# Kernel tuning notes

Hardware: AMD Instinct MI355X
Metric: run time of the kernel (lower is better)

## Reference

```python
import jax, jax.numpy as jnp
import numpy as np

B, L, C, H = 8, 16384, 128, 4
EPS = 1e-5


def setup_inputs() -> dict:
    key = jax.random.key(0)
    k1, k2, k3, k4 = jax.random.split(key, 4)
    return {
        "x": jax.random.normal(k1, (B, L, C), dtype=jnp.float32),
        "W_qkv": jax.random.normal(k2, (3 * C, C), dtype=jnp.float32) * (C ** -0.5),
        "W_out": jax.random.normal(k3, (C, C), dtype=jnp.float32) * (C ** -0.5),
        "b_out": jax.random.normal(k4, (C,), dtype=jnp.float32) * 0.01,
        "gn_w": jnp.ones((C,), dtype=jnp.float32),
        "gn_b": jnp.zeros((C,), dtype=jnp.float32),
    }


def reference(x, W_qkv, W_out, b_out, gn_w, gn_b):
    b, l, c = x.shape
    h = H
    d = c // h                      # dim_head
    scale = d ** -0.5
    xc = jnp.swapaxes(x, 1, 2)      # [b, c, l]
    # 1x1 conv == channel matmul
    qkv = jnp.einsum('oc,bcl->bol', W_qkv, xc)     # [b, 3c, l]
    q, k, v = jnp.split(qkv, 3, axis=1)
    q = q.reshape(b, h, d, l)
    k = k.reshape(b, h, d, l)
    v = v.reshape(b, h, d, l)
    q = jax.nn.softmax(q, axis=2) * scale          # softmax over head-dim
    k = jax.nn.softmax(k, axis=3)                  # softmax over length
    context = jnp.einsum('bhcj,bhdj->bhcd', k, v)  # [b, h, d, d]
    out = jnp.einsum('bhcd,bhdi->bhci', context, q)  # [b, h, d, l]
    out = out.reshape(b, h * d, l)
    out = jnp.einsum('oc,bcl->bol', W_out, out) + b_out[None, :, None]
    # GroupNorm(1, c): normalize over (channel, length) per sample
    mean = jnp.mean(out, axis=(1, 2), keepdims=True)
    var = jnp.var(out, axis=(1, 2), keepdims=True)
    out = (out - mean) * jax.lax.rsqrt(var + EPS)
    out = out * gn_w[None, :, None] + gn_b[None, :, None]
    return jnp.swapaxes(out, 1, 2)                 # [b, l, c]
```

## Files before the change

### kernel.cpp

```cpp
#include <hip/hip_runtime.h>

#define BATCH 8
#define SEQL 16384
#define NCH 128
#define NH 4
#define HD 32
#define GEPS 1e-5f

typedef __bf16 bf16x8 __attribute__((ext_vector_type(8)));
typedef __bf16 bf16x4 __attribute__((ext_vector_type(4)));
typedef float f32x4 __attribute__((ext_vector_type(4)));

#define WKV_B   0
#define WQ_B    65536
#define WO_B    98304
#define CTXB_B  131072
#define GNS_B   196608
#define CTXP_B  262144


__global__ void k_prep(const float* __restrict__ wqkv, const float* __restrict__ wout,
                       char* __restrict__ wsb) {
    int i = blockIdx.x * 256 + threadIdx.x;
    __bf16* wkvb = (__bf16*)(wsb + WKV_B);
    __bf16* wqb  = (__bf16*)(wsb + WQ_B);
    __bf16* wob  = (__bf16*)(wsb + WO_B);
    if (i < 384 * 128) {
        int o = i >> 7, c = i & 127;
        __bf16 v = (__bf16)wqkv[i];
        if (o < 128) wqb[o * 128 + c] = v;
        else         wkvb[(o - 128) * 128 + c] = v;
    }
    if (i < 128 * 128) wob[i] = (__bf16)wout[i];
    if (i < 16) ((float*)(wsb + GNS_B))[i] = 0.f;
}

__global__ __launch_bounds__(256, 4) void k_pass1(const float* __restrict__ x,
                                                  char* __restrict__ wsb, int P) {
    __shared__ __attribute__((aligned(16))) __bf16 xb[8352];
    __shared__ __attribute__((aligned(16))) __bf16 ekv[8232];
    const int t = threadIdx.x;
    const int lane = t & 63, wave = t >> 6;
    const int n16 = lane & 15, q = lane >> 4;
    const int batch = blockIdx.x / P, sub = blockIdx.x % P;
    const int nrep = 256 / P;
    const __bf16* __restrict__ wkvb = (const __bf16*)(wsb + WKV_B);

    f32x4 ctxacc[2][2];
#pragma unroll
    for (int i = 0; i < 2; i++)
#pragma unroll
        for (int j = 0; j < 2; j++) ctxacc[i][j] = (f32x4){0.f, 0.f, 0.f, 0.f};
    float zacc[2][4];
#pragma unroll
    for (int i = 0; i < 2; i++)
#pragma unroll
        for (int j = 0; j < 4; j++) zacc[i][j] = 0.f;

    for (int rep = 0; rep < nrep; rep++) {
        const int chunk = sub + rep * P;
        const float* xg = x + (size_t)(batch * SEQL + chunk * 64) * NCH;
#pragma unroll
        for (int r = 0; r < 8; r++) {
            int e = t + r * 256;
            int tok = e >> 5, c4 = (e & 31) * 4;
            float4 v = ((const float4*)xg)[e];
            bf16x4 h; h.x = (__bf16)v.x; h.y = (__bf16)v.y; h.z = (__bf16)v.z; h.w = (__bf16)v.w;
            *(bf16x4*)&xb[(c4 >> 5) * 2088 + ((c4 >> 3) & 3) * 520 + tok * 8 + (c4 & 7)] = h;
        }
        __syncthreads();

#pragma unroll
        for (int half = 0; half < 2; half++) {
            f32x4 kvacc[4][2];
#pragma unroll
            for (int i = 0; i < 4; i++)
#pragma unroll
                for (int j = 0; j < 2; j++) kvacc[i][j] = (f32x4){0.f, 0.f, 0.f, 0.f};
#pragma unroll
            for (int ks = 0; ks < 4; ks++) {
                bf16x8 aw_k[4];
#pragma unroll
                for (int mt = 0; mt < 4; mt++)
                    aw_k[mt] = *(const bf16x8*)&wkvb[(mt * 64 + wave * 16 + n16) * 128 + ks * 32 + q * 8];
                bf16x8 b[2];
#pragma unroll
                for (int nl = 0; nl < 2; nl++)
                    b[nl] = *(const bf16x8*)&xb[ks * 2088 + q * 520 + ((half * 2 + nl) * 16 + n16) * 8];
#pragma unroll
                for (int mt = 0; mt < 4; mt++)
#pragma unroll
                    for (int nl = 0; nl < 2; nl++)
                        kvacc[mt][nl] = __builtin_amdgcn_mfma_f32_16x16x32_bf16(
                            aw_k[mt], b[nl], kvacc[mt][nl], 0, 0, 0);
            }
#pragma unroll
            for (int mt = 0; mt < 4; mt++)
#pragma unroll
                for (int nl = 0; nl < 2; nl++) {
                    int ti = nl * 16 + n16;
                    int base = (ti >> 3) * 2056 + (ti & 7);
#pragma unroll
                    for (int r = 0; r < 4; r++) {
                        float vv = kvacc[mt][nl][r];
                        if (mt < 2) { vv = __expf(vv); zacc[mt][r] += vv; }
                        int o = mt * 64 + wave * 16 + q * 4 + r;
                        ekv[base + o * 8] = (__bf16)vv;
                    }
                }
            __syncthreads();
            {
                bf16x8 ea[2], vb[2];
#pragma unroll
                for (int ml = 0; ml < 2; ml++) {
                    ea[ml] = *(const bf16x8*)&ekv[q * 2056 + (wave * 32 + ml * 16 + n16) * 8];
                    vb[ml] = *(const bf16x8*)&ekv[q * 2056 + (128 + wave * 32 + ml * 16 + n16) * 8];
                }
#pragma unroll
                for (int ml = 0; ml < 2; ml++)
#pragma unroll
                    for (int nl = 0; nl < 2; nl++)
                        ctxacc[ml][nl] = __builtin_amdgcn_mfma_f32_16x16x32_bf16(
                            ea[ml], vb[nl], ctxacc[ml][nl], 0, 0, 0);
            }
            if (half == 0) __syncthreads();
        }
    }

    float* ctxp = (float*)(wsb + CTXP_B) + (size_t)blockIdx.x * 4096 + wave * 1024;
#pragma unroll
    for (int nl = 0; nl < 2; nl++)
#pragma unroll
        for (int ml = 0; ml < 2; ml++) {
            float4 v4;
            v4.x = ctxacc[ml][nl][0]; v4.y = ctxacc[ml][nl][1];
            v4.z = ctxacc[ml][nl][2]; v4.w = ctxacc[ml][nl][3];
            *(float4*)&ctxp[(nl * 16 + n16) * 32 + ml * 16 + q * 4] = v4;
        }
    {
        float* zpT = (float*)(wsb + CTXP_B) + (size_t)BATCH * P * 4096;
#pragma unroll
        for (int mt = 0; mt < 2; mt++)
#pragma unroll
            for (int r = 0; r < 4; r++) {
                float z = zacc[mt][r];
                z += __shfl_xor(z, 1); z += __shfl_xor(z, 2);
                z += __shfl_xor(z, 4); z += __shfl_xor(z, 8);
                if (n16 == 0)
                    zpT[((size_t)batch * 128 + mt * 64 + wave * 16 + q * 4 + r) * P + sub] = z;
            }
    }
}

__global__ __launch_bounds__(256) void k_reduce(char* __restrict__ wsb, int P) {
    __shared__ float red[4][64];
    __shared__ float zw[32];
    const int tid = threadIdx.x;
    const int b = blockIdx.x >> 6, eg = blockIdx.x & 63;
    const float* ctxp = (const float*)(wsb + CTXP_B);
    const float* zpT = ctxp + (size_t)BATCH * P * 4096;

    {
        int ci = tid >> 3, pslot = tid & 7;
        size_t row = ((size_t)b * 128 + (size_t)(eg >> 4) * 32 + ci) * P;
        float zs = 0.f;
        for (int p = pslot; p < P; p += 8) zs += zpT[row + p];
        zs += __shfl_xor(zs, 1); zs += __shfl_xor(zs, 2); zs += __shfl_xor(zs, 4);
        if (pslot == 0) zw[ci] = zs;
    }
    {
        int pg = tid >> 6, e = tid & 63;
        int cnt = P >> 2;
        const float* base = ctxp + ((size_t)(b * P + pg * cnt)) * 4096 + eg * 64 + e;
        float cs = 0.f;
        for (int k = 0; k < cnt; k++) cs += base[(size_t)k * 4096];
        red[pg][e] = cs;
    }
    __syncthreads();
    if (tid < 64) {
        float tot = red[0][tid] + red[1][tid] + red[2][tid] + red[3][tid];
        int e = eg * 64 + tid;
        int h = e >> 10, d = (e >> 5) & 31, c = e & 31;
        ((__bf16*)(wsb + CTXB_B))[((size_t)b << 12) + (h << 10) + (c << 5) + d] =
            (__bf16)(tot / zw[c]);
    }
}

__global__ __launch_bounds__(256, 4) void k_pass2(const float* __restrict__ x,
                                                  const float* __restrict__ bout,
                                                  char* __restrict__ wsb,
                                                  float* __restrict__ out) {
    __shared__ __attribute__((aligned(16))) __bf16 xb[8352];
    __shared__ __attribute__((aligned(16))) __bf16 pB[8352];
    __shared__ float gred[8];
    const int t = threadIdx.x;
    const int lane = t & 63, wave = t >> 6;
    const int n16 = lane & 15, q = lane >> 4;
    const int batch = blockIdx.x >> 7, sub = blockIdx.x & 127;
    const __bf16* __restrict__ wqb = (const __bf16*)(wsb + WQ_B);
    const __bf16* __restrict__ wob = (const __bf16*)(wsb + WO_B);
    const __bf16* __restrict__ ctxb = (const __bf16*)(wsb + CTXB_B);

    bf16x8 actx[2];
#pragma unroll
    for (int ml = 0; ml < 2; ml++)
        actx[ml] = *(const bf16x8*)&ctxb[((size_t)(batch * 4 + wave) * 32 + ml * 16 + n16) * 32 + q * 8];
    float4 bias[2];
#pragma unroll
    for (int ml = 0; ml < 2; ml++)
        bias[ml] = *(const float4*)&bout[wave * 32 + ml * 16 + q * 4];

    {
        const float* xg = x + (size_t)(batch * SEQL + sub * 64) * NCH;
#pragma unroll
        for (int r = 0; r < 8; r++) {
            int e = t + r * 256;
            int tok = e >> 5, c4 = (e & 31) * 4;
            float4 v = ((const float4*)xg)[e];
            bf16x4 h; h.x = (__bf16)v.x; h.y = (__bf16)v.y; h.z = (__bf16)v.z; h.w = (__bf16)v.w;
            *(bf16x4*)&xb[(c4 >> 5) * 2088 + ((c4 >> 3) & 3) * 520 + tok * 8 + (c4 & 7)] = h;
        }
    }

    float s1 = 0.f, s2 = 0.f;
    bf16x4 hpre[8];

#pragma unroll
    for (int rep = 0; rep < 2; rep++) {
        const int chunk = sub + rep * 128;
        const size_t tok0 = (size_t)batch * SEQL + chunk * 64;
        __syncthreads();
        f32x4 qacc[2][4];
#pragma unroll
        for (int i = 0; i < 2; i++)
#pragma unroll
            for (int j = 0; j < 4; j++) qacc[i][j] = (f32x4){0.f, 0.f, 0.f, 0.f};
#pragma unroll
        for (int ks = 0; ks < 4; ks++) {
            bf16x8 aq_k[2];
#pragma unroll
            for (int ml = 0; ml < 2; ml++)
                aq_k[ml] = *(const bf16x8*)&wqb[(wave * 32 + ml * 16 + n16) * 128 + ks * 32 + q * 8];
            bf16x8 b[4];
#pragma unroll
            for (int nt = 0; nt < 4; nt++)
                b[nt] = *(const bf16x8*)&xb[ks * 2088 + q * 520 + (nt * 16 + n16) * 8];
#pragma unroll
            for (int ml = 0; ml < 2; ml++)
#pragma unroll
                for (int nt = 0; nt < 4; nt++)
                    qacc[ml][nt] = __builtin_amdgcn_mfma_f32_16x16x32_bf16(
                        aq_k[ml], b[nt], qacc[ml][nt], 0, 0, 0);
        }
        float4 vpre[8];
        if (rep == 0) {
            const float* xg2 = x + (size_t)(batch * SEQL + (sub + 128) * 64) * NCH;
#pragma unroll
            for (int r = 0; r < 8; r++) vpre[r] = ((const float4*)xg2)[t + r * 256];
        }
#pragma unroll
        for (int nt = 0; nt < 4; nt++) {
            float ss = 0.f;
#pragma unroll
            for (int ml = 0; ml < 2; ml++)
#pragma unroll
                for (int r = 0; r < 4; r++) {
                    float e = __expf(qacc[ml][nt][r]);
                    qacc[ml][nt][r] = e;
                    ss += e;
                }
            ss += __shfl_xor(ss, 16);
            ss += __shfl_xor(ss, 32);
            float inv = 0.17677669529663687f / ss;
#pragma unroll
            for (int ml = 0; ml < 2; ml++)
#pragma unroll
                for (int r = 0; r < 4; r++) qacc[ml][nt][r] *= inv;
        }
#pragma unroll
        for (int ml = 0; ml < 2; ml++)
#pragma unroll
            for (int nt = 0; nt < 4; nt++) {
                bf16x4 h;
                h.x = (__bf16)qacc[ml][nt][0]; h.y = (__bf16)qacc[ml][nt][1];
                h.z = (__bf16)qacc[ml][nt][2]; h.w = (__bf16)qacc[ml][nt][3];
                *(bf16x4*)&pB[wave * 2088 + (ml * 2 + (q >> 1)) * 520 +
                              (nt * 16 + n16) * 8 + (q & 1) * 4] = h;
            }
        __syncthreads();
        f32x4 aacc[2][4];
#pragma unroll
        for (int ml = 0; ml < 2; ml++)
#pragma unroll
            for (int nt = 0; nt < 4; nt++) {
                bf16x8 pb = *(const bf16x8*)&pB[wave * 2088 + q * 520 + (nt * 16 + n16) * 8];
                aacc[ml][nt] = __builtin_amdgcn_mfma_f32_16x16x32_bf16(
                    actx[ml], pb, (f32x4){0.f, 0.f, 0.f, 0.f}, 0, 0, 0);
            }
        if (rep == 0) {
#pragma unroll
            for (int r = 0; r < 8; r++) {
                bf16x4 h;
                h.x = (__bf16)vpre[r].x; h.y = (__bf16)vpre[r].y;
                h.z = (__bf16)vpre[r].z; h.w = (__bf16)vpre[r].w;
                hpre[r] = h;
            }
        }
        __bf16* attB = xb;
#pragma unroll
        for (int ml = 0; ml < 2; ml++)
#pragma unroll
            for (int nt = 0; nt < 4; nt++) {
                bf16x4 h;
                h.x = (__bf16)aacc[ml][nt][0]; h.y = (__bf16)aacc[ml][nt][1];
                h.z = (__bf16)aacc[ml][nt][2]; h.w = (__bf16)aacc[ml][nt][3];
                *(bf16x4*)&attB[wave * 2088 + (ml * 2 + (q >> 1)) * 520 +
                                (nt * 16 + n16) * 8 + (q & 1) * 4] = h;
            }
        __syncthreads();
        f32x4 oacc[2][4];
#pragma unroll
        for (int i = 0; i < 2; i++)
#pragma unroll
            for (int j = 0; j < 4; j++) oacc[i][j] = (f32x4){0.f, 0.f, 0.f, 0.f};
#pragma unroll
        for (int ks = 0; ks < 4; ks++) {
            bf16x8 ao_k[2];
#pragma unroll
            for (int ml = 0; ml < 2; ml++)
                ao_k[ml] = *(const bf16x8*)&wob[(wave * 32 + ml * 16 + n16) * 128 + ks * 32 + q * 8];
            bf16x8 b[4];
#pragma unroll
            for (int nt = 0; nt < 4; nt++)
                b[nt] = *(const bf16x8*)&attB[ks * 2088 + q * 520 + (nt * 16 + n16) * 8];
#pragma unroll
            for (int ml = 0; ml < 2; ml++)
#pragma unroll
                for (int nt = 0; nt < 4; nt++)
                    oacc[ml][nt] = __builtin_amdgcn_mfma_f32_16x16x32_bf16(
                        ao_k[ml], b[nt], oacc[ml][nt], 0, 0, 0);
        }
#pragma unroll
        for (int ml = 0; ml < 2; ml++)
#pragma unroll
            for (int nt = 0; nt < 4; nt++) {
                float4 vv;
                vv.x = oacc[ml][nt][0] + bias[ml].x;
                vv.y = oacc[ml][nt][1] + bias[ml].y;
                vv.z = oacc[ml][nt][2] + bias[ml].z;
                vv.w = oacc[ml][nt][3] + bias[ml].w;
                s1 += vv.x + vv.y + vv.z + vv.w;
                s2 += vv.x * vv.x + vv.y * vv.y + vv.z * vv.z + vv.w * vv.w;
                *(float4*)&out[(tok0 + nt * 16 + n16) * NCH + wave * 32 + ml * 16 + q * 4] = vv;
            }
        if (rep == 0) {
            __syncthreads();
#pragma unroll
            for (int r = 0; r < 8; r++) {
                int e = t + r * 256;
                int tok = e >> 5, c4 = (e & 31) * 4;
                *(bf16x4*)&xb[(c4 >> 5) * 2088 + ((c4 >> 3) & 3) * 520 + tok * 8 + (c4 & 7)] = hpre[r];
            }
        }
    }
#pragma unroll
    for (int off = 32; off > 0; off >>= 1) {
        s1 += __shfl_xor(s1, off);
        s2 += __shfl_xor(s2, off);
    }
    if (lane == 0) { gred[wave * 2 + 0] = s1; gred[wave * 2 + 1] = s2; }
    __syncthreads();
    if (t < 2) {
        float s = gred[t] + gred[2 + t] + gred[4 + t] + gred[6 + t];
        atomicAdd(&((float*)(wsb + GNS_B))[batch * 2 + t], s);
    }
}

__global__ __launch_bounds__(256) void k_gnorm(float* __restrict__ out,
                                               const char* __restrict__ wsb,
                                               const float* __restrict__ gw,
                                               const float* __restrict__ gb) {
    size_t base4 = ((size_t)blockIdx.x * 256 + threadIdx.x) * 2;
    int b = (int)(base4 >> 19);
    const float* gns = (const float*)(wsb + GNS_B);
    const float n = (float)NCH * (float)SEQL;
    float mean = gns[b * 2] / n;
    float var = gns[b * 2 + 1] / n - mean * mean;
    float rstd = rsqrtf(var + GEPS);
    int cbase = (int)((base4 & 31) * 4);
    float4 w0 = *(const float4*)&gw[cbase];
    float4 w1 = *(const float4*)&gw[cbase + 4];
    float4 b0 = *(const float4*)&gb[cbase];
    float4 b1 = *(const float4*)&gb[cbase + 4];
    float4 v0 = ((float4*)out)[base4];
    float4 v1 = ((float4*)out)[base4 + 1];
    v0.x = (v0.x - mean) * rstd * w0.x + b0.x;
    v0.y = (v0.y - mean) * rstd * w0.y + b0.y;
    v0.z = (v0.z - mean) * rstd * w0.z + b0.z;
    v0.w = (v0.w - mean) * rstd * w0.w + b0.w;
    v1.x = (v1.x - mean) * rstd * w1.x + b1.x;
    v1.y = (v1.y - mean) * rstd * w1.y + b1.y;
    v1.z = (v1.z - mean) * rstd * w1.z + b1.z;
    v1.w = (v1.w - mean) * rstd * w1.w + b1.w;
    ((float4*)out)[base4] = v0;
    ((float4*)out)[base4 + 1] = v1;
}

extern "C" void kernel_launch(void* const* d_in, const int* in_sizes, int n_in,
                              void* d_out, int out_size, void* d_ws, size_t ws_size,
                              hipStream_t stream) {
    const float* x    = (const float*)d_in[0];
    const float* wqkv = (const float*)d_in[1];
    const float* wout = (const float*)d_in[2];
    const float* bout = (const float*)d_in[3];
    const float* gw   = (const float*)d_in[4];
    const float* gb   = (const float*)d_in[5];
    float* out = (float*)d_out;
    char* wsb  = (char*)d_ws;

    int P = 256;
    while (P > 4 &&
           (size_t)CTXP_B + (size_t)BATCH * P * (16384 + 512) > ws_size)
        P >>= 1;

    k_prep<<<192, 256, 0, stream>>>(wqkv, wout, wsb);
    k_pass1<<<BATCH * P, 256, 0, stream>>>(x, wsb, P);
    k_reduce<<<BATCH * 64, 256, 0, stream>>>(wsb, P);
    k_pass2<<<1024, 256, 0, stream>>>(x, bout, wsb, out);
    k_gnorm<<<8192, 256, 0, stream>>>(out, wsb, gw, gb);
}
```

Before: 245.8 us.

## Fuse GroupNorm into pass2 via cooperative grid sync; prefetch x in pass1

Measured after the change: 494.6 us. 101% more time.

```diff
diff --git a/kernel.cpp b/kernel.cpp
--- a/kernel.cpp
+++ b/kernel.cpp
@@ -1,4 +1,7 @@
 #include <hip/hip_runtime.h>
+#include <hip/hip_cooperative_groups.h>
+
+namespace cg = cooperative_groups;
 
 #define BATCH 8
 #define SEQL 16384
@@ -57,9 +60,8 @@
 #pragma unroll
         for (int j = 0; j < 4; j++) zacc[i][j] = 0.f;
 
-    for (int rep = 0; rep < nrep; rep++) {
-        const int chunk = sub + rep * P;
-        const float* xg = x + (size_t)(batch * SEQL + chunk * 64) * NCH;
+    {
+        const float* xg = x + (size_t)(batch * SEQL + sub * 64) * NCH;
 #pragma unroll
         for (int r = 0; r < 8; r++) {
             int e = t + r * 256;
@@ -68,10 +70,20 @@
             bf16x4 h; h.x = (__bf16)v.x; h.y = (__bf16)v.y; h.z = (__bf16)v.z; h.w = (__bf16)v.w;
             *(bf16x4*)&xb[(c4 >> 5) * 2088 + ((c4 >> 3) & 3) * 520 + tok * 8 + (c4 & 7)] = h;
         }
+    }
+
+    for (int rep = 0; rep < nrep; rep++) {
         __syncthreads();
+        float4 vpre[8];
+        const bool hasNext = (rep + 1 < nrep);
 
 #pragma unroll
         for (int half = 0; half < 2; half++) {
+            if (half == 1 && hasNext) {
+                const float* xg2 = x + (size_t)(batch * SEQL + (sub + (rep + 1) * P) * 64) * NCH;
+#pragma unroll
+                for (int r = 0; r < 8; r++) vpre[r] = ((const float4*)xg2)[t + r * 256];
+            }
             f32x4 kvacc[4][2];
 #pragma unroll
             for (int i = 0; i < 4; i++)
@@ -125,6 +137,17 @@
             }
             if (half == 0) __syncthreads();
         }
+        if (hasNext) {
+#pragma unroll
+            for (int r = 0; r < 8; r++) {
+                int e = t + r * 256;
+                int tok = e >> 5, c4 = (e & 31) * 4;
+                bf16x4 h;
+                h.x = (__bf16)vpre[r].x; h.y = (__bf16)vpre[r].y;
+                h.z = (__bf16)vpre[r].z; h.w = (__bf16)vpre[r].w;
+                *(bf16x4*)&xb[(c4 >> 5) * 2088 + ((c4 >> 3) & 3) * 520 + tok * 8 + (c4 & 7)] = h;
+            }
+        }
     }
 
     float* ctxp = (float*)(wsb + CTXP_B) + (size_t)blockIdx.x * 4096 + wave * 1024;
@@ -138,7 +161,7 @@
             *(float4*)&ctxp[(nl * 16 + n16) * 32 + ml * 16 + q * 4] = v4;
         }
     {
-        float* zpT = (float*)(wsb + CTXP_B) + (size_t)BATCH * P * 4096;
+        float* zp = (float*)(wsb + CTXP_B) + (size_t)BATCH * P * 4096 + (size_t)blockIdx.x * 128;
 #pragma unroll
         for (int mt = 0; mt < 2; mt++)
 #pragma unroll
@@ -146,27 +169,26 @@
                 float z = zacc[mt][r];
                 z += __shfl_xor(z, 1); z += __shfl_xor(z, 2);
                 z += __shfl_xor(z, 4); z += __shfl_xor(z, 8);
-                if (n16 == 0)
-                    zpT[((size_t)batch * 128 + mt * 64 + wave * 16 + q * 4 + r) * P + sub] = z;
+                if (n16 == 0) zp[mt * 64 + wave * 16 + q * 4 + r] = z;
             }
     }
 }
 
 __global__ __launch_bounds__(256) void k_reduce(char* __restrict__ wsb, int P) {
     __shared__ float red[4][64];
-    __shared__ float zw[32];
+    __shared__ float zred[8][33];
     const int tid = threadIdx.x;
     const int b = blockIdx.x >> 6, eg = blockIdx.x & 63;
     const float* ctxp = (const float*)(wsb + CTXP_B);
-    const float* zpT = ctxp + (size_t)BATCH * P * 4096;
+    const float* zp = ctxp + (size_t)BATCH * P * 4096;
 
     {
-        int ci = tid >> 3, pslot = tid & 7;
-        size_t row = ((size_t)b * 128 + (size_t)(eg >> 4) * 32 + ci) * P;
+        int ci = tid & 31, pslot = tid >> 5;
+        int ho = (eg >> 4) * 32;
         float zs = 0.f;
-        for (int p = pslot; p < P; p += 8) zs += zpT[row + p];
-        zs += __shfl_xor(zs, 1); zs += __shfl_xor(zs, 2); zs += __shfl_xor(zs, 4);
-        if (pslot == 0) zw[ci] = zs;
+        for (int p = pslot; p < P; p += 8)
+            zs += zp[(size_t)(b * P + p) * 128 + ho + ci];
+        zred[pslot][ci] = zs;
     }
     {
         int pg = tid >> 6, e = tid & 63;
@@ -179,17 +201,24 @@
     __syncthreads();
     if (tid < 64) {
         float tot = red[0][tid] + red[1][tid] + red[2][tid] + red[3][tid];
+        int c = tid & 31;
+        float zs = 0.f;
+#pragma unroll
+        for (int s = 0; s < 8; s++) zs += zred[s][c];
         int e = eg * 64 + tid;
-        int h = e >> 10, d = (e >> 5) & 31, c = e & 31;
+        int h = e >> 10, d = (e >> 5) & 31;
         ((__bf16*)(wsb + CTXB_B))[((size_t)b << 12) + (h << 10) + (c << 5) + d] =
-            (__bf16)(tot / zw[c]);
+            (__bf16)(tot / zs);
     }
 }
 
 __global__ __launch_bounds__(256, 4) void k_pass2(const float* __restrict__ x,
                                                   const float* __restrict__ bout,
+                                                  const float* __restrict__ gw,
+                                                  const float* __restrict__ gb,
                                                   char* __restrict__ wsb,
-                                                  float* __restrict__ out) {
+                                                  float* __restrict__ out,
+                                                  int fused) {
     __shared__ __attribute__((aligned(16))) __bf16 xb[8352];
     __shared__ __attribute__((aligned(16))) __bf16 pB[8352];
     __shared__ float gred[8];
@@ -224,6 +253,7 @@
 
     float s1 = 0.f, s2 = 0.f;
     bf16x4 hpre[8];
+    f32x4 held[2][4];
 
 #pragma unroll
     for (int rep = 0; rep < 2; rep++) {
@@ -351,7 +381,12 @@
                 vv.w = oacc[ml][nt][3] + bias[ml].w;
                 s1 += vv.x + vv.y + vv.z + vv.w;
                 s2 += vv.x * vv.x + vv.y * vv.y + vv.z * vv.z + vv.w * vv.w;
-                *(float4*)&out[(tok0 + nt * 16 + n16) * NCH + wave * 32 + ml * 16 + q * 4] = vv;
+                if (rep == 0 || !fused) {
+                    *(float4*)&out[(tok0 + nt * 16 + n16) * NCH + wave * 32 + ml * 16 + q * 4] = vv;
+                } else {
+                    held[ml][nt][0] = vv.x; held[ml][nt][1] = vv.y;
+                    held[ml][nt][2] = vv.z; held[ml][nt][3] = vv.w;
+                }
             }
         if (rep == 0) {
             __syncthreads();
@@ -373,6 +408,48 @@
     if (t < 2) {
         float s = gred[t] + gred[2 + t] + gred[4 + t] + gred[6 + t];
         atomicAdd(&((float*)(wsb + GNS_B))[batch * 2 + t], s);
+    }
+
+    if (fused) {
+        __threadfence();
+        cg::this_grid().sync();
+        const float* gns = (const float*)(wsb + GNS_B);
+        const float n = (float)NCH * (float)SEQL;
+        float mean = gns[batch * 2] / n;
+        float var = gns[batch * 2 + 1] / n - mean * mean;
+        float rstd = rsqrtf(var + GEPS);
+        {
+            float4 w4 = *(const float4*)&gw[(t & 31) * 4];
+            float4 b4 = *(const float4*)&gb[(t & 31) * 4];
+            float4* out4 = (float4*)out;
+            size_t base = ((size_t)batch * SEQL + (size_t)sub * 64) * 32;
+#pragma unroll
+            for (int j = 0; j < 8; j++) {
+                float4 v = out4[base + j * 256 + t];
+                v.x = (v.x - mean) * rstd * w4.x + b4.x;
+                v.y = (v.y - mean) * rstd * w4.y + b4.y;
+                v.z = (v.z - mean) * rstd * w4.z + b4.z;
+                v.w = (v.w - mean) * rstd * w4.w + b4.w;
+                out4[base + j * 256 + t] = v;
+            }
+        }
+        {
+            const size_t tok1 = (size_t)batch * SEQL + (size_t)(sub + 128) * 64;
+#pragma unroll
+            for (int ml = 0; ml < 2; ml++) {
+                float4 wg = *(const float4*)&gw[wave * 32 + ml * 16 + q * 4];
+                float4 bg = *(const float4*)&gb[wave * 32 + ml * 16 + q * 4];
+#pragma unroll
+                for (int nt = 0; nt < 4; nt++) {
+                    float4 v;
+                    v.x = (held[ml][nt][0] - mean) * rstd * wg.x + bg.x;
+                    v.y = (held[ml][nt][1] - mean) * rstd * wg.y + bg.y;
+                    v.z = (held[ml][nt][2] - mean) * rstd * wg.z + bg.z;
+                    v.w = (held[ml][nt][3] - mean) * rstd * wg.w + bg.w;
+                    *(float4*)&out[(tok1 + nt * 16 + n16) * NCH + wave * 32 + ml * 16 + q * 4] = v;
+                }
+            }
+        }
     }
 }
 
@@ -418,7 +495,7 @@
     float* out = (float*)d_out;
     char* wsb  = (char*)d_ws;
 
-    int P = 256;
+    int P = 128;
     while (P > 4 &&
            (size_t)CTXP_B + (size_t)BATCH * P * (16384 + 512) > ws_size)
         P >>= 1;
@@ -426,6 +503,24 @@
     k_prep<<<192, 256, 0, stream>>>(wqkv, wout, wsb);
     k_pass1<<<BATCH * P, 256, 0, stream>>>(x, wsb, P);
     k_reduce<<<BATCH * 64, 256, 0, stream>>>(wsb, P);
-    k_pass2<<<1024, 256, 0, stream>>>(x, bout, wsb, out);
-    k_gnorm<<<8192, 256, 0, stream>>>(out, wsb, gw, gb);
+
+    static int coop = -1;
+    if (coop < 0) {
+        int v = 0;
+        if (hipDeviceGetAttribute(&v, hipDeviceAttributeCooperativeLaunch, 0) != hipSuccess) v = 0;
+        coop = v;
+    }
+    bool fusedDone = false;
+    if (coop) {
+        int fused = 1;
+        void* args[] = {(void*)&x, (void*)&bout, (void*)&gw, (void*)&gb,
+                        (void*)&wsb, (void*)&out, (void*)&fused};
+        if (hipLaunchCooperativeKernel((const void*)k_pass2, dim3(1024), dim3(256),
+                                       args, 0, stream) == hipSuccess)
+            fusedDone = true;
+    }
+    if (!fusedDone) {
+        k_pass2<<<1024, 256, 0, stream>>>(x, bout, gw, gb, wsb, out, 0);
+        k_gnorm<<<8192, 256, 0, stream>>>(out, wsb, gw, gb);
+    }
 }
```

## Prefetch next x chunk in pass1, hoist pass2 weights, coalesce z partials, halve P

Applied to the files above, without the earlier changes.

After: 264.7 us. 1.08x slower.

```diff
diff --git a/kernel.cpp b/kernel.cpp
--- a/kernel.cpp
+++ b/kernel.cpp
@@ -57,9 +57,8 @@
 #pragma unroll
         for (int j = 0; j < 4; j++) zacc[i][j] = 0.f;
 
-    for (int rep = 0; rep < nrep; rep++) {
-        const int chunk = sub + rep * P;
-        const float* xg = x + (size_t)(batch * SEQL + chunk * 64) * NCH;
+    {
+        const float* xg = x + (size_t)(batch * SEQL + sub * 64) * NCH;
 #pragma unroll
         for (int r = 0; r < 8; r++) {
             int e = t + r * 256;
@@ -68,10 +67,20 @@
             bf16x4 h; h.x = (__bf16)v.x; h.y = (__bf16)v.y; h.z = (__bf16)v.z; h.w = (__bf16)v.w;
             *(bf16x4*)&xb[(c4 >> 5) * 2088 + ((c4 >> 3) & 3) * 520 + tok * 8 + (c4 & 7)] = h;
         }
+    }
+
+    for (int rep = 0; rep < nrep; rep++) {
         __syncthreads();
+        float4 vpre[8];
+        const bool hasNext = (rep + 1 < nrep);
 
 #pragma unroll
         for (int half = 0; half < 2; half++) {
+            if (half == 1 && hasNext) {
+                const float* xg2 = x + (size_t)(batch * SEQL + (sub + (rep + 1) * P) * 64) * NCH;
+#pragma unroll
+                for (int r = 0; r < 8; r++) vpre[r] = ((const float4*)xg2)[t + r * 256];
+            }
             f32x4 kvacc[4][2];
 #pragma unroll
             for (int i = 0; i < 4; i++)
@@ -125,6 +134,17 @@
             }
             if (half == 0) __syncthreads();
         }
+        if (hasNext) {
+#pragma unroll
+            for (int r = 0; r < 8; r++) {
+                int e = t + r * 256;
+                int tok = e >> 5, c4 = (e & 31) * 4;
+                bf16x4 h;
+                h.x = (__bf16)vpre[r].x; h.y = (__bf16)vpre[r].y;
+                h.z = (__bf16)vpre[r].z; h.w = (__bf16)vpre[r].w;
+                *(bf16x4*)&xb[(c4 >> 5) * 2088 + ((c4 >> 3) & 3) * 520 + tok * 8 + (c4 & 7)] = h;
+            }
+        }
     }
 
     float* ctxp = (float*)(wsb + CTXP_B) + (size_t)blockIdx.x * 4096 + wave * 1024;
@@ -138,7 +158,7 @@
             *(float4*)&ctxp[(nl * 16 + n16) * 32 + ml * 16 + q * 4] = v4;
         }
     {
-        float* zpT = (float*)(wsb + CTXP_B) + (size_t)BATCH * P * 4096;
+        float* zp = (float*)(wsb + CTXP_B) + (size_t)BATCH * P * 4096 + (size_t)blockIdx.x * 128;
 #pragma unroll
         for (int mt = 0; mt < 2; mt++)
 #pragma unroll
@@ -146,27 +166,26 @@
                 float z = zacc[mt][r];
                 z += __shfl_xor(z, 1); z += __shfl_xor(z, 2);
                 z += __shfl_xor(z, 4); z += __shfl_xor(z, 8);
-                if (n16 == 0)
-                    zpT[((size_t)batch * 128 + mt * 64 + wave * 16 + q * 4 + r) * P + sub] = z;
+                if (n16 == 0) zp[mt * 64 + wave * 16 + q * 4 + r] = z;
             }
     }
 }
 
 __global__ __launch_bounds__(256) void k_reduce(char* __restrict__ wsb, int P) {
     __shared__ float red[4][64];
-    __shared__ float zw[32];
+    __shared__ float zred[8][33];
     const int tid = threadIdx.x;
     const int b = blockIdx.x >> 6, eg = blockIdx.x & 63;
     const float* ctxp = (const float*)(wsb + CTXP_B);
-    const float* zpT = ctxp + (size_t)BATCH * P * 4096;
+    const float* zp = ctxp + (size_t)BATCH * P * 4096;
 
     {
-        int ci = tid >> 3, pslot = tid & 7;
-        size_t row = ((size_t)b * 128 + (size_t)(eg >> 4) * 32 + ci) * P;
+        int ci = tid & 31, pslot = tid >> 5;
+        int ho = (eg >> 4) * 32;
         float zs = 0.f;
-        for (int p = pslot; p < P; p += 8) zs += zpT[row + p];
-        zs += __shfl_xor(zs, 1); zs += __shfl_xor(zs, 2); zs += __shfl_xor(zs, 4);
-        if (pslot == 0) zw[ci] = zs;
+        for (int p = pslot; p < P; p += 8)
+            zs += zp[(size_t)(b * P + p) * 128 + ho + ci];
+        zred[pslot][ci] = zs;
     }
     {
         int pg = tid >> 6, e = tid & 63;
@@ -179,10 +198,14 @@
     __syncthreads();
     if (tid < 64) {
         float tot = red[0][tid] + red[1][tid] + red[2][tid] + red[3][tid];
+        int c = tid & 31;
+        float zs = 0.f;
+#pragma unroll
+        for (int s = 0; s < 8; s++) zs += zred[s][c];
         int e = eg * 64 + tid;
-        int h = e >> 10, d = (e >> 5) & 31, c = e & 31;
+        int h = e >> 10, d = (e >> 5) & 31;
         ((__bf16*)(wsb + CTXB_B))[((size_t)b << 12) + (h << 10) + (c << 5) + d] =
-            (__bf16)(tot / zw[c]);
+            (__bf16)(tot / zs);
     }
 }
 
@@ -201,6 +224,14 @@
     const __bf16* __restrict__ wob = (const __bf16*)(wsb + WO_B);
     const __bf16* __restrict__ ctxb = (const __bf16*)(wsb + CTXB_B);
 
+    bf16x8 aq[2][4], ao[2][4];
+#pragma unroll
+    for (int ml = 0; ml < 2; ml++)
+#pragma unroll
+        for (int ks = 0; ks < 4; ks++) {
+            aq[ml][ks] = *(const bf16x8*)&wqb[(wave * 32 + ml * 16 + n16) * 128 + ks * 32 + q * 8];
+            ao[ml][ks] = *(const bf16x8*)&wob[(wave * 32 + ml * 16 + n16) * 128 + ks * 32 + q * 8];
+        }
     bf16x8 actx[2];
 #pragma unroll
     for (int ml = 0; ml < 2; ml++)
@@ -237,10 +268,6 @@
             for (int j = 0; j < 4; j++) qacc[i][j] = (f32x4){0.f, 0.f, 0.f, 0.f};
 #pragma unroll
         for (int ks = 0; ks < 4; ks++) {
-            bf16x8 aq_k[2];
-#pragma unroll
-            for (int ml = 0; ml < 2; ml++)
-                aq_k[ml] = *(const bf16x8*)&wqb[(wave * 32 + ml * 16 + n16) * 128 + ks * 32 + q * 8];
             bf16x8 b[4];
 #pragma unroll
             for (int nt = 0; nt < 4; nt++)
@@ -250,7 +277,7 @@
 #pragma unroll
                 for (int nt = 0; nt < 4; nt++)
                     qacc[ml][nt] = __builtin_amdgcn_mfma_f32_16x16x32_bf16(
-                        aq_k[ml], b[nt], qacc[ml][nt], 0, 0, 0);
+                        aq[ml][ks], b[nt], qacc[ml][nt], 0, 0, 0);
         }
         float4 vpre[8];
         if (rep == 0) {
@@ -325,10 +352,6 @@
             for (int j = 0; j < 4; j++) oacc[i][j] = (f32x4){0.f, 0.f, 0.f, 0.f};
 #pragma unroll
         for (int ks = 0; ks < 4; ks++) {
-            bf16x8 ao_k[2];
-#pragma unroll
-            for (int ml = 0; ml < 2; ml++)
-                ao_k[ml] = *(const bf16x8*)&wob[(wave * 32 + ml * 16 + n16) * 128 + ks * 32 + q * 8];
             bf16x8 b[4];
 #pragma unroll
             for (int nt = 0; nt < 4; nt++)
@@ -338,7 +361,7 @@
 #pragma unroll
                 for (int nt = 0; nt < 4; nt++)
                     oacc[ml][nt] = __builtin_amdgcn_mfma_f32_16x16x32_bf16(
-                        ao_k[ml], b[nt], oacc[ml][nt], 0, 0, 0);
+                        ao[ml][ks], b[nt], oacc[ml][nt], 0, 0, 0);
         }
 #pragma unroll
         for (int ml = 0; ml < 2; ml++)
@@ -418,7 +441,7 @@
     float* out = (float*)d_out;
     char* wsb  = (char*)d_ws;
 
-    int P = 256;
+    int P = 128;
     while (P > 4 &&
            (size_t)CTXP_B + (size_t)BATCH * P * (16384 + 512) > ws_size)
         P >>= 1;
```
